# Performance work log

Measured on AMD Instinct MI355X. Metric: run time of the kernel, lower is better.

The kernel has to match this reference:

```python
import jax, jax.numpy as jnp
import numpy as np

B, T, F, U = 256, 2048, 64, 10  # batch, timesteps, features, lstm units


def setup_inputs() -> dict:
    key = jax.random.key(0)
    k1, k2, k3, k4 = jax.random.split(key, 4)
    return {
        "x": jax.random.normal(k1, (B, T, F), dtype=jnp.float32),
        "kernel": jax.random.normal(k2, (F, 4 * U), dtype=jnp.float32) * 0.1,
        "recurrent_kernel": jax.random.normal(k3, (U, 4 * U), dtype=jnp.float32) * 0.1,
        "bias": jnp.zeros((4 * U,), dtype=jnp.float32),
        "dense_w": jax.random.normal(k4, (U, 1), dtype=jnp.float32) * 0.1,
        "dense_b": jnp.zeros((1,), dtype=jnp.float32),
    }


def reference(x, kernel, recurrent_kernel, bias, dense_w, dense_b):
    units = recurrent_kernel.shape[0]
    batch = x.shape[0]
    # Precompute input contribution for all timesteps: [B, T, 4U]
    xz = jnp.einsum('btf,fg->btg', x, kernel) + bias

    def step(carry, z_t):
        h, c = carry
        z = z_t + h @ recurrent_kernel  # [B, 4U]
        i, f, g, o = jnp.split(z, 4, axis=-1)  # Keras gate order: i, f, c, o
        i = jax.nn.sigmoid(i)
        f = jax.nn.sigmoid(f)
        g = jax.nn.soft_sign(g)       # activation='softsign'
        o = jax.nn.sigmoid(o)
        c = f * c + i * g
        h = o * jax.nn.soft_sign(c)
        return (h, c), None

    h0 = jnp.zeros((batch, units), dtype=x.dtype)
    (h, _), _ = jax.lax.scan(step, (h0, h0), jnp.swapaxes(xz, 0, 1))
    logit = h @ dense_w + dense_b  # [B, 1]
    return jax.nn.sigmoid(logit)
```

## Files before the change

### kernel.cpp

```cpp
#include <hip/hip_runtime.h>

#define B_ 256
#define T_ 2048
#define F_ 64
#define U_ 10
#define G_ 40
#define CH 64
#define NCH (T_ / CH)

__device__ __forceinline__ float rcp_f(float x) { return __builtin_amdgcn_rcpf(x); }
__device__ __forceinline__ float rdlane_f(float v, int l) {
  return __int_as_float(__builtin_amdgcn_readlane(__float_as_int(v), l));
}
template <int CTRL>
__device__ __forceinline__ float qbcast(float v) {
  return __int_as_float(
      __builtin_amdgcn_update_dpp(0, __float_as_int(v), CTRL, 0xF, 0xF, true));
}
__device__ __forceinline__ void gload_lds16(const float* g, float* l) {
  __builtin_amdgcn_global_load_lds(
      (const __attribute__((address_space(1))) void*)g,
      (__attribute__((address_space(3))) void*)l, 16, 0, 0);
}

__global__ __launch_bounds__(256, 1) void lstm_fused(
    const float* __restrict__ x, const float* __restrict__ W,
    const float* __restrict__ R, const float* __restrict__ bias,
    const float* __restrict__ dw, const float* __restrict__ db,
    float* __restrict__ out) {
  __shared__ float xb[2][CH * F_];
  __shared__ float zb[2][CH * G_];
  const int b = blockIdx.x;
  const int tid = threadIdx.x;
  const int wave = tid >> 6;
  const int lane = tid & 63;
  const float* xbase = x + (size_t)b * T_ * F_;

  if (wave == 0) {
    __builtin_amdgcn_s_setprio(3);
    const int L = (lane < G_) ? lane : (G_ - 1);
    const int u = L >> 2, gate = L & 3;
    const int col = gate * U_ + u;
    float Rc[U_];
    #pragma unroll
    for (int j = 0; j < U_; ++j) Rc[j] = R[j * G_ + col];
    const float dwu = dw[u];
    const float db0 = db[0];
    float h = 0.f, c = 0.f;
    __syncthreads();
    __syncthreads();
    for (int cc = 0; cc < NCH; ++cc) {
      const float* zrow = zb[cc & 1] + L;
      float zpf[4];
      #pragma unroll
      for (int k = 0; k < 4; ++k) zpf[k] = zrow[k * G_];
      for (int t0 = 0; t0 < CH; t0 += 4) {
        #pragma unroll
        for (int k = 0; k < 4; ++k) {
          float z0 = zpf[k];
          int tn = t0 + 4 + k;
          if (tn > CH - 1) tn = CH - 1;
          zpf[k] = zrow[tn * G_];
          float z1 = 0.f;
          #pragma unroll
          for (int j = 0; j < U_; j += 2) {
            float ha = rdlane_f(h, 4 * j);
            float hb = rdlane_f(h, 4 * (j + 1));
            z0 = fmaf(ha, Rc[j], z0);
            z1 = fmaf(hb, Rc[j + 1], z1);
          }
          float zz = z0 + z1;
          float sg = rcp_f(1.f + __expf(-zz));
          float ss = zz * rcp_f(1.f + __builtin_fabsf(zz));
          float a = (gate == 2) ? ss : sg;
          float ai = qbcast<0x00>(a);
          float af = qbcast<0x55>(a);
          float ag = qbcast<0xAA>(a);
          float ao = qbcast<0xFF>(a);
          c = fmaf(af, c, ai * ag);
          float oc = ao * c;
          float den = 1.f + __builtin_fabsf(c);
          h = oc * rcp_f(den);
        }
      }
      __syncthreads();
    }
    float p = h * dwu;
    float logit = db0;
    #pragma unroll
    for (int j = 0; j < U_; ++j) logit += rdlane_f(p, 4 * j);
    if (lane == 0) out[b] = rcp_f(1.f + __expf(-logit));
  } else {
    const int p0 = tid - 64;
    const int p = (p0 < 160) ? p0 : 159;
    const bool act = (p0 < 160);
    const int s = p % G_;
    const int tsl = p / G_;
    const int u = s >> 2, gate = s & 3;
    const int col = gate * U_ + u;
    const int pw = wave - 1;
    float wc[F_];
    #pragma unroll
    for (int k = 0; k < F_; ++k) wc[k] = W[k * G_ + col];
    const float bcol = bias[col];

    auto load_x = [&](int cx) {
      const float* g = xbase + (size_t)cx * CH * F_;
      float* l = xb[cx & 1];
      for (int i = pw; i < 16; i += 3)
        gload_lds16(g + i * 256 + lane * 4, l + i * 256);
    };
    auto produce = [&](int tc) {
      const float* xr = xb[tc & 1];
      float* zrow = zb[tc & 1];
      for (int tt = tsl; tt < CH; tt += 4) {
        const float4* row4 = (const float4*)(xr + tt * F_);
        float z0 = bcol, z1 = 0.f, z2 = 0.f, z3 = 0.f;
        #pragma unroll
        for (int j = 0; j < 16; j += 4) {
          float4 a0 = row4[j], a1 = row4[j + 1], a2 = row4[j + 2], a3 = row4[j + 3];
          z0 = fmaf(a0.x, wc[4*j+0], z0);  z0 = fmaf(a0.y, wc[4*j+1], z0);
          z0 = fmaf(a0.z, wc[4*j+2], z0);  z0 = fmaf(a0.w, wc[4*j+3], z0);
          z1 = fmaf(a1.x, wc[4*j+4], z1);  z1 = fmaf(a1.y, wc[4*j+5], z1);
          z1 = fmaf(a1.z, wc[4*j+6], z1);  z1 = fmaf(a1.w, wc[4*j+7], z1);
          z2 = fmaf(a2.x, wc[4*j+8], z2);  z2 = fmaf(a2.y, wc[4*j+9], z2);
          z2 = fmaf(a2.z, wc[4*j+10], z2); z2 = fmaf(a2.w, wc[4*j+11], z2);
          z3 = fmaf(a3.x, wc[4*j+12], z3); z3 = fmaf(a3.y, wc[4*j+13], z3);
          z3 = fmaf(a3.z, wc[4*j+14], z3); z3 = fmaf(a3.w, wc[4*j+15], z3);
        }
        if (act) zrow[tt * G_ + s] = (z0 + z1) + (z2 + z3);
      }
    };

    load_x(0);
    load_x(1);
    __syncthreads();
    produce(0);
    __syncthreads();
    for (int cc = 0; cc < NCH; ++cc) {
      if (cc + 2 < NCH) load_x(cc + 2);
      if (cc + 1 < NCH) produce(cc + 1);
      __syncthreads();
    }
  }
}

extern "C" void kernel_launch(void* const* d_in, const int* in_sizes, int n_in,
                              void* d_out, int out_size, void* d_ws, size_t ws_size,
                              hipStream_t stream) {
  const float* x    = (const float*)d_in[0];
  const float* W    = (const float*)d_in[1];
  const float* R    = (const float*)d_in[2];
  const float* bias = (const float*)d_in[3];
  const float* dw   = (const float*)d_in[4];
  const float* db   = (const float*)d_in[5];
  float* out = (float*)d_out;
  (void)d_ws; (void)ws_size; (void)in_sizes; (void)n_in; (void)out_size;
  lstm_fused<<<B_, 256, 0, stream>>>(x, W, R, bias, dw, db, out);
}
```

Baseline: 355.6 us.

## Prescale gate weights by -log2e, halve chunk size, and batch z loads as float2

The sigmoid gate pre-activations are pre-multiplied by -log2(e) in both the recurrent weights and the producer output, so the serial step uses a raw exp2 with no extra multiply. The chunk shrinks from 64 to 32 timesteps, the z buffer is stored as float2 pairs of consecutive timesteps, and all 16 pairs of a chunk are loaded into registers up front. This removes per-step LDS prefetch bookkeeping from the latency-bound recurrent loop. In exchange there are twice as many block barriers and more register pressure in the fully unrolled recurrent loop.

```diff
diff --git a/kernel.cpp b/kernel.cpp
--- a/kernel.cpp
+++ b/kernel.cpp
@@ -5,10 +5,13 @@
 #define F_ 64
 #define U_ 10
 #define G_ 40
-#define CH 64
+#define CH 32
+#define CH2 (CH / 2)
 #define NCH (T_ / CH)
+#define NLOG2E (-1.44269504088896340736f)
 
 __device__ __forceinline__ float rcp_f(float x) { return __builtin_amdgcn_rcpf(x); }
+__device__ __forceinline__ float exp2_f(float x) { return __builtin_amdgcn_exp2f(x); }
 __device__ __forceinline__ float rdlane_f(float v, int l) {
   return __int_as_float(__builtin_amdgcn_readlane(__float_as_int(v), l));
 }
@@ -29,7 +32,7 @@
     const float* __restrict__ dw, const float* __restrict__ db,
     float* __restrict__ out) {
   __shared__ float xb[2][CH * F_];
-  __shared__ float zb[2][CH * G_];
+  __shared__ float2 zb[2][CH2 * G_];
   const int b = blockIdx.x;
   const int tid = threadIdx.x;
   const int wave = tid >> 6;
@@ -41,47 +44,51 @@
     const int L = (lane < G_) ? lane : (G_ - 1);
     const int u = L >> 2, gate = L & 3;
     const int col = gate * U_ + u;
+    const float sc = (gate == 2) ? 1.f : NLOG2E;
     float Rc[U_];
     #pragma unroll
-    for (int j = 0; j < U_; ++j) Rc[j] = R[j * G_ + col];
+    for (int j = 0; j < U_; ++j) Rc[j] = R[j * G_ + col] * sc;
     const float dwu = dw[u];
     const float db0 = db[0];
     float h = 0.f, c = 0.f;
+
+    auto step = [&](float zseed) {
+      float h0 = rdlane_f(h, 0),  h1 = rdlane_f(h, 4),  h2 = rdlane_f(h, 8);
+      float h3 = rdlane_f(h, 12), h4 = rdlane_f(h, 16), h5 = rdlane_f(h, 20);
+      float h6 = rdlane_f(h, 24), h7 = rdlane_f(h, 28);
+      float h8 = rdlane_f(h, 32), h9 = rdlane_f(h, 36);
+      float z0 = fmaf(h0, Rc[0], zseed);
+      float z1 = h1 * Rc[1];
+      z0 = fmaf(h2, Rc[2], z0);  z1 = fmaf(h3, Rc[3], z1);
+      z0 = fmaf(h4, Rc[4], z0);  z1 = fmaf(h5, Rc[5], z1);
+      z0 = fmaf(h6, Rc[6], z0);  z1 = fmaf(h7, Rc[7], z1);
+      z0 = fmaf(h8, Rc[8], z0);  z1 = fmaf(h9, Rc[9], z1);
+      float zz = z0 + z1;
+      float e = exp2_f(zz);
+      float t = (gate == 2) ? __builtin_fabsf(zz) : e;
+      float r = rcp_f(1.f + t);
+      float a = (gate == 2) ? zz * r : r;
+      float ai = qbcast<0x00>(a);
+      float af = qbcast<0x55>(a);
+      float ag = qbcast<0xAA>(a);
+      float ao = qbcast<0xFF>(a);
+      c = fmaf(af, c, ai * ag);
+      float oc = ao * c;
+      float den = 1.f + __builtin_fabsf(c);
+      h = oc * rcp_f(den);
+    };
+
     __syncthreads();
     __syncthreads();
     for (int cc = 0; cc < NCH; ++cc) {
-      const float* zrow = zb[cc & 1] + L;
-      float zpf[4];
+      const float2* zp = zb[cc & 1] + L;
+      float2 sd[CH2];
       #pragma unroll
-      for (int k = 0; k < 4; ++k) zpf[k] = zrow[k * G_];
-      for (int t0 = 0; t0 < CH; t0 += 4) {
-        #pragma unroll
-        for (int k = 0; k < 4; ++k) {
-          float z0 = zpf[k];
-          int tn = t0 + 4 + k;
-          if (tn > CH - 1) tn = CH - 1;
-          zpf[k] = zrow[tn * G_];
-          float z1 = 0.f;
-          #pragma unroll
-          for (int j = 0; j < U_; j += 2) {
-            float ha = rdlane_f(h, 4 * j);
-            float hb = rdlane_f(h, 4 * (j + 1));
-            z0 = fmaf(ha, Rc[j], z0);
-            z1 = fmaf(hb, Rc[j + 1], z1);
-          }
-          float zz = z0 + z1;
-          float sg = rcp_f(1.f + __expf(-zz));
-          float ss = zz * rcp_f(1.f + __builtin_fabsf(zz));
-          float a = (gate == 2) ? ss : sg;
-          float ai = qbcast<0x00>(a);
-          float af = qbcast<0x55>(a);
-          float ag = qbcast<0xAA>(a);
-          float ao = qbcast<0xFF>(a);
-          c = fmaf(af, c, ai * ag);
-          float oc = ao * c;
-          float den = 1.f + __builtin_fabsf(c);
-          h = oc * rcp_f(den);
-        }
+      for (int k = 0; k < CH2; ++k) sd[k] = zp[k * G_];
+      #pragma unroll
+      for (int k = 0; k < CH2; ++k) {
+        step(sd[k].x);
+        step(sd[k].y);
       }
       __syncthreads();
     }
@@ -95,10 +102,11 @@
     const int p = (p0 < 160) ? p0 : 159;
     const bool act = (p0 < 160);
     const int s = p % G_;
-    const int tsl = p / G_;
+    const int tp = p / G_;
     const int u = s >> 2, gate = s & 3;
     const int col = gate * U_ + u;
     const int pw = wave - 1;
+    const float scp = (gate == 2) ? 1.f : NLOG2E;
     float wc[F_];
     #pragma unroll
     for (int k = 0; k < F_; ++k) wc[k] = W[k * G_ + col];
@@ -107,28 +115,35 @@
     auto load_x = [&](int cx) {
       const float* g = xbase + (size_t)cx * CH * F_;
       float* l = xb[cx & 1];
-      for (int i = pw; i < 16; i += 3)
+      for (int i = pw; i < 8; i += 3)
         gload_lds16(g + i * 256 + lane * 4, l + i * 256);
+    };
+    auto dot = [&](const float* xr) -> float {
+      const float4* row4 = (const float4*)xr;
+      float z0 = bcol, z1 = 0.f, z2 = 0.f, z3 = 0.f;
+      #pragma unroll
+      for (int j = 0; j < 16; j += 4) {
+        float4 a0 = row4[j], a1 = row4[j + 1], a2 = row4[j + 2], a3 = row4[j + 3];
+        z0 = fmaf(a0.x, wc[4*j+0], z0);  z0 = fmaf(a0.y, wc[4*j+1], z0);
+        z0 = fmaf(a0.z, wc[4*j+2], z0);  z0 = fmaf(a0.w, wc[4*j+3], z0);
+        z1 = fmaf(a1.x, wc[4*j+4], z1);  z1 = fmaf(a1.y, wc[4*j+5], z1);
+        z1 = fmaf(a1.z, wc[4*j+6], z1);  z1 = fmaf(a1.w, wc[4*j+7], z1);
+        z2 = fmaf(a2.x, wc[4*j+8], z2);  z2 = fmaf(a2.y, wc[4*j+9], z2);
+        z2 = fmaf(a2.z, wc[4*j+10], z2); z2 = fmaf(a2.w, wc[4*j+11], z2);
+        z3 = fmaf(a3.x, wc[4*j+12], z3); z3 = fmaf(a3.y, wc[4*j+13], z3);
+        z3 = fmaf(a3.z, wc[4*j+14], z3); z3 = fmaf(a3.w, wc[4*j+15], z3);
+      }
+      return ((z0 + z1) + (z2 + z3)) * scp;
     };
     auto produce = [&](int tc) {
       const float* xr = xb[tc & 1];
-      float* zrow = zb[tc & 1];
-      for (int tt = tsl; tt < CH; tt += 4) {
-        const float4* row4 = (const float4*)(xr + tt * F_);
-        float z0 = bcol, z1 = 0.f, z2 = 0.f, z3 = 0.f;
-        #pragma unroll
-        for (int j = 0; j < 16; j += 4) {
-          float4 a0 = row4[j], a1 = row4[j + 1], a2 = row4[j + 2], a3 = row4[j + 3];
-          z0 = fmaf(a0.x, wc[4*j+0], z0);  z0 = fmaf(a0.y, wc[4*j+1], z0);
-          z0 = fmaf(a0.z, wc[4*j+2], z0);  z0 = fmaf(a0.w, wc[4*j+3], z0);
-          z1 = fmaf(a1.x, wc[4*j+4], z1);  z1 = fmaf(a1.y, wc[4*j+5], z1);
-          z1 = fmaf(a1.z, wc[4*j+6], z1);  z1 = fmaf(a1.w, wc[4*j+7], z1);
-          z2 = fmaf(a2.x, wc[4*j+8], z2);  z2 = fmaf(a2.y, wc[4*j+9], z2);
-          z2 = fmaf(a2.z, wc[4*j+10], z2); z2 = fmaf(a2.w, wc[4*j+11], z2);
-          z3 = fmaf(a3.x, wc[4*j+12], z3); z3 = fmaf(a3.y, wc[4*j+13], z3);
-          z3 = fmaf(a3.z, wc[4*j+14], z3); z3 = fmaf(a3.w, wc[4*j+15], z3);
-        }
-        if (act) zrow[tt * G_ + s] = (z0 + z1) + (z2 + z3);
+      float2* zrow = zb[tc & 1];
+      #pragma unroll
+      for (int k = 0; k < 4; ++k) {
+        const int t2 = tp + 4 * k;
+        float zE = dot(xr + (2 * t2) * F_);
+        float zO = dot(xr + (2 * t2 + 1) * F_);
+        if (act) zrow[t2 * G_ + s] = make_float2(zE, zO);
       }
     };
 
```

Result: faster. 337.2 us (-5.2%).
